# Kernel tuning notes

Measured on AMD Instinct MI355X. Metric: run time of the kernel, lower is better.

## Reference

```python
import jax, jax.numpy as jnp
import numpy as np

N = 50000      # nodes
E = 800000     # edges (before self loops)
NF = 4         # node feature dim
EF = 4         # edge feature dim
EMB = 16       # joint embedding dim
HID = 64       # hidden dim
OUT = 128      # output dim
H = 4          # heads (layers 0,1); last layer has 1 head
NEG_SLOPE = 0.2


def setup_inputs() -> dict:
    key = jax.random.key(0)
    ks = jax.random.split(key, 20)
    in0 = NF + EMB  # 20

    def lin(k, o, i):
        return (jax.random.normal(k, (o, i), jnp.float32) * np.float32(1.0 / np.sqrt(i)))

    return {
        'x': jax.random.normal(ks[0], (N, NF), jnp.float32),
        'edge_index': jax.random.randint(ks[1], (2, E), 0, N, dtype=jnp.int32),
        'edge_attr': jax.random.normal(ks[2], (E, EF), jnp.float32),
        'joint_types': jax.random.randint(ks[3], (N,), 0, 17, dtype=jnp.int32),
        'emb_table': jax.random.normal(ks[4], (17, EMB), jnp.float32) * 0.1,
        'W0': lin(ks[5], H * HID, in0),
        'a_src0': jax.random.normal(ks[6], (H, HID), jnp.float32) * 0.1,
        'a_dst0': jax.random.normal(ks[7], (H, HID), jnp.float32) * 0.1,
        'We0': lin(ks[8], H, EF),
        'W1': lin(ks[9], H * HID, HID),
        'a_src1': jax.random.normal(ks[10], (H, HID), jnp.float32) * 0.1,
        'a_dst1': jax.random.normal(ks[11], (H, HID), jnp.float32) * 0.1,
        'We1': lin(ks[12], H, EF),
        'W2': lin(ks[13], 1 * OUT, HID),
        'a_src2': jax.random.normal(ks[14], (1, OUT), jnp.float32) * 0.1,
        'a_dst2': jax.random.normal(ks[15], (1, OUT), jnp.float32) * 0.1,
        'We2': lin(ks[16], 1, EF),
    }


def gat_layer(x, src, dst, eattr, W, a_src, a_dst, We, num_nodes):
    # x: [N, F_in]; W: [H*C, F_in]; a_src/a_dst: [H, C]; We: [H, EF]
    Hh, C = a_src.shape
    h = (x @ W.T).reshape(num_nodes, Hh, C)  # [N, H, C]
    # per-node attention scores, gathered per edge (same math as per-edge dot)
    s_i = jnp.einsum('nhc,hc->nh', h, a_src)  # applied to x_i = x[dst]
    s_j = jnp.einsum('nhc,hc->nh', h, a_dst)  # applied to x_j = x[src]
    alpha = s_i[dst] + s_j[src] + eattr @ We.T  # [Etot, H]
    alpha = jax.nn.leaky_relu(alpha, NEG_SLOPE)
    # faithful to torch.softmax(alpha, dim=0): GLOBAL softmax over all edges per head
    alpha = jax.nn.softmax(alpha, axis=0)
    msgs = h[src] * alpha[:, :, None]  # [Etot, H, C]
    out = jax.ops.segment_sum(msgs, dst, num_segments=num_nodes)  # aggr='add'
    return out.mean(axis=1)  # update(): mean over heads -> [N, C]


def reference(x, edge_index, edge_attr, joint_types, emb_table,
              W0, a_src0, a_dst0, We0,
              W1, a_src1, a_dst1, We1,
              W2, a_src2, a_dst2, We2):
    num_nodes = x.shape[0]
    # add self loops (edge_attr fill 0.0)
    loops = jnp.arange(num_nodes, dtype=edge_index.dtype)
    src = jnp.concatenate([edge_index[0], loops])
    dst = jnp.concatenate([edge_index[1], loops])
    eattr = jnp.concatenate([edge_attr, jnp.zeros((num_nodes, edge_attr.shape[1]), edge_attr.dtype)], axis=0)

    h = jnp.concatenate([x, emb_table[joint_types]], axis=-1)  # [N, 20]
    h = gat_layer(h, src, dst, eattr, W0, a_src0, a_dst0, We0, num_nodes)
    h = jax.nn.elu(h)  # dropout is identity in eval mode
    h = gat_layer(h, src, dst, eattr, W1, a_src1, a_dst1, We1, num_nodes)
    h = jax.nn.elu(h)
    h = gat_layer(h, src, dst, eattr, W2, a_src2, a_dst2, We2, num_nodes)
    return h  # [N, OUT]
```

## Files before the change

kernel.cpp:

```cpp
#include <hip/hip_runtime.h>
#include <math.h>

#define NN 50000
#define EE 800000
#define EEN (EE+NN)
#define STRIDE 64
#define NFEAT 4
#define EFEAT 4
#define EMBD 16
#define IN0 20
#define HIDD 64
#define OUTD 128
#define EDGE_NB 1024

__device__ __forceinline__ unsigned short f2bf(float f){
  unsigned u = __float_as_uint(f);
  return (unsigned short)((u + 0x7FFFu + ((u>>16)&1u)) >> 16);
}
__device__ __forceinline__ float bfl(unsigned u){ return __uint_as_float(u<<16); }
__device__ __forceinline__ float bfh(unsigned u){ return __uint_as_float(u & 0xFFFF0000u); }

__device__ __forceinline__ unsigned f2h2(float a, float b){
  _Float16 ha=(_Float16)a, hb=(_Float16)b;
  unsigned short ua=*(unsigned short*)&ha, ub=*(unsigned short*)&hb;
  return (unsigned)ua | ((unsigned)ub<<16);
}
__device__ __forceinline__ float h2f(unsigned short u){
  _Float16 h=*(_Float16*)&u; return (float)h;
}

typedef unsigned uv4 __attribute__((ext_vector_type(4)));
typedef unsigned uv2 __attribute__((ext_vector_type(2)));
template<typename T>
__device__ __forceinline__ T ntload(const T* p){
  return __builtin_nontemporal_load(const_cast<T*>(p));
}

template<int V> struct ldt;
template<> struct ldt<4>{ using T = uint2; };
template<> struct ldt<2>{ using T = unsigned int; };

template<int F_IN,int HH,int CC>
__device__ __forceinline__ void av_one(const float* W, const float* asrc,
                                       const float* adst, float* av, int tid){
  if (tid >= HH*F_IN) return;
  int h = tid / F_IN, f = tid % F_IN;
  float s1=0.f, s2=0.f;
  for (int c=0;c<CC;c++){
    float wv = W[(size_t)(h*CC+c)*F_IN+f];
    s1 += asrc[h*CC+c]*wv;
    s2 += adst[h*CC+c]*wv;
  }
  av[tid] = s1;
  av[HH*F_IN+tid] = s2;
}
__global__ void k_av3(const float* W0, const float* as0, const float* ad0, float* av0,
                      const float* W1, const float* as1, const float* ad1, float* av1,
                      const float* W2, const float* as2, const float* ad2, float* av2,
                      float* zred, int* fill){
  int b = blockIdx.x, tid = threadIdx.x;
  if      (b==0){ av_one<IN0,4,64> (W0, as0, ad0, av0, tid); if (tid<192) zred[tid]=0.f; }
  else if (b==1)  av_one<64,4,64>  (W1, as1, ad1, av1, tid);
  else if (b==2)  av_one<64,1,128> (W2, as2, ad2, av2, tid);
  else { int i=(b-3)*256+tid; if (i<NN) fill[i]=0; }
}

__global__ void k_scatter(const int* __restrict__ ei, const float4* __restrict__ eattr,
                          int* fill, uv4* __restrict__ erec){
  int idx = blockIdx.x*blockDim.x + threadIdx.x;
  if (idx < EE){
    int d = ei[EE+idx];
    int s = ei[idx];
    float4 ea = eattr[idx];
    int pos = atomicAdd(&fill[d],1);
    int slot = d*STRIDE + 1 + pos;
    uv4 r; r.x=(unsigned)s; r.y=f2h2(ea.x,ea.y); r.z=f2h2(ea.z,ea.w); r.w=0u;
    erec[slot]=r;
  } else if (idx < EEN){
    int n = idx-EE;
    uv4 r; r.x=(unsigned)n; r.y=0u; r.z=0u; r.w=0u;
    erec[n*STRIDE]=r;
  }
}

template<int K,int NCOL,int HH,bool CONCAT>
__global__ __launch_bounds__(256)
void k_gemm(const float* __restrict__ xin, const int* __restrict__ jt,
            const float* __restrict__ emb, const float* __restrict__ W,
            const float* __restrict__ avp, unsigned short* __restrict__ hout,
            float* __restrict__ si, float* __restrict__ sj){
  constexpr int PITCH = 132;
  __shared__ float xT[K*PITCH];
  __shared__ float wT[K*PITCH];
  __shared__ float EMBL[CONCAT ? 17*EMBD : 1];
  int tid = threadIdx.x;
  int rbase = blockIdx.x*128, cbase = blockIdx.y*128;
  if (CONCAT){
    for (int i=tid; i<17*EMBD; i+=256) EMBL[i]=emb[i];
    __syncthreads();
    if (tid < 128){
      int row = tid;
      int gr = rbase+row; if (gr >= NN) gr = NN-1;
      float4 v = ((const float4*)xin)[gr];
      xT[0*PITCH+row]=v.x; xT[1*PITCH+row]=v.y;
      xT[2*PITCH+row]=v.z; xT[3*PITCH+row]=v.w;
      int j = jt[gr];
      #pragma unroll
      for (int k=0;k<EMBD;k++) xT[(NFEAT+k)*PITCH+row] = EMBL[j*EMBD+k];
    } else {
      int col = tid-128;
      const float4* wp = (const float4*)(W + (size_t)(cbase+col)*K);
      #pragma unroll
      for (int k4=0;k4<K/4;k4++){
        float4 v = wp[k4];
        wT[(4*k4+0)*PITCH+col]=v.x; wT[(4*k4+1)*PITCH+col]=v.y;
        wT[(4*k4+2)*PITCH+col]=v.z; wT[(4*k4+3)*PITCH+col]=v.w;
      }
    }
  } else {
    constexpr int K4 = K/4;
    for (int i=tid; i<128*K4; i+=256){
      int row = i/K4, k4 = i%K4;
      int gr = rbase+row; if (gr >= NN) gr = NN-1;
      float4 v = ((const float4*)xin)[(size_t)gr*K4 + k4];
      xT[(4*k4+0)*PITCH+row]=v.x; xT[(4*k4+1)*PITCH+row]=v.y;
      xT[(4*k4+2)*PITCH+row]=v.z; xT[(4*k4+3)*PITCH+row]=v.w;
    }
    for (int i=tid; i<128*K4; i+=256){
      int col = i/K4, k4 = i%K4;
      float4 v = ((const float4*)W)[(size_t)(cbase+col)*K4 + k4];
      wT[(4*k4+0)*PITCH+col]=v.x; wT[(4*k4+1)*PITCH+col]=v.y;
      wT[(4*k4+2)*PITCH+col]=v.z; wT[(4*k4+3)*PITCH+col]=v.w;
    }
  }
  __syncthreads();
  int lane = tid & 63, w = tid >> 6;
  int r0 = (w>>1)*64 + (lane&7)*8;
  int c0 = (w&1)*64 + (lane>>3)*8;
  float acc[8][8];
  #pragma unroll
  for (int i=0;i<8;i++)
    #pragma unroll
    for (int j=0;j<8;j++) acc[i][j]=0.f;
  #pragma unroll 4
  for (int k=0;k<K;k++){
    float a[8], b[8];
    *(float4*)&a[0] = *(const float4*)&xT[k*PITCH + r0];
    *(float4*)&a[4] = *(const float4*)&xT[k*PITCH + r0 + 4];
    *(float4*)&b[0] = *(const float4*)&wT[k*PITCH + c0];
    *(float4*)&b[4] = *(const float4*)&wT[k*PITCH + c0 + 4];
    #pragma unroll
    for (int i=0;i<8;i++)
      #pragma unroll
      for (int j=0;j<8;j++) acc[i][j] += a[i]*b[j];
  }
  if (blockIdx.y==0 && tid < 128){
    int row = tid, gr = rbase+row;
    if (gr < NN){
      #pragma unroll
      for (int h=0;h<HH;h++){
        float a=0.f, b=0.f;
        for (int k=0;k<K;k++){
          float xv = xT[k*PITCH+row];
          a += xv*avp[h*K+k];
          b += xv*avp[HH*K+h*K+k];
        }
        si[(size_t)gr*HH+h]=a;
        sj[(size_t)gr*HH+h]=b;
      }
    }
  }
  #pragma unroll
  for (int i=0;i<8;i++){
    int n = rbase + r0 + i;
    if (n < NN){
      uint4 o;
      o.x = (unsigned)f2bf(acc[i][0]) | ((unsigned)f2bf(acc[i][1])<<16);
      o.y = (unsigned)f2bf(acc[i][2]) | ((unsigned)f2bf(acc[i][3])<<16);
      o.z = (unsigned)f2bf(acc[i][4]) | ((unsigned)f2bf(acc[i][5])<<16);
      o.w = (unsigned)f2bf(acc[i][6]) | ((unsigned)f2bf(acc[i][7])<<16);
      *(uint4*)(hout + (size_t)n*NCOL + cbase + c0) = o;
    }
  }
}

template<int HH>
__global__ __launch_bounds__(256)
void k_edge2(const uv4* __restrict__ erec, const int* __restrict__ fill,
             const float* __restrict__ We, const float* __restrict__ si,
             const float* __restrict__ sj, unsigned* __restrict__ prec,
             float* __restrict__ zred){
  int wave = threadIdx.x>>6, lane = threadIdx.x&63;
  float z[HH];
  #pragma unroll
  for (int h=0;h<HH;h++) z[h]=0.f;
  for (int n = blockIdx.x*4 + wave; n < NN; n += EDGE_NB*4){
    int cnt = 1 + fill[n];
    if (lane < cnt){
      int slot = n*STRIDE + lane;
      uv4 r = ntload(&erec[slot]);
      int s = (int)r.x;
      float eax=h2f((unsigned short)(r.y&0xFFFFu)), eay=h2f((unsigned short)(r.y>>16));
      float eaz=h2f((unsigned short)(r.z&0xFFFFu)), eaw=h2f((unsigned short)(r.z>>16));
      if constexpr (HH==4){
        float4 siv = ((const float4*)si)[n];
        float4 sjv = ((const float4*)sj)[s];
        float te[4] = {siv.x+sjv.x, siv.y+sjv.y, siv.z+sjv.z, siv.w+sjv.w};
        float pv[4];
        #pragma unroll
        for (int h=0;h<4;h++){
          float t = te[h] + eax*We[h*EFEAT+0] + eay*We[h*EFEAT+1]
                          + eaz*We[h*EFEAT+2] + eaw*We[h*EFEAT+3];
          t = (t>0.f)? t : 0.2f*t;
          float p = expf(t);
          z[h]+=p; pv[h]=p;
        }
        uv4 o; o.x=f2h2(pv[0],pv[1]); o.y=f2h2(pv[2],pv[3]); o.z=(unsigned)s; o.w=0u;
        ((uv4*)prec)[slot] = o;
      } else {
        float t = si[n] + sj[s]
                + eax*We[0] + eay*We[1] + eaz*We[2] + eaw*We[3];
        t = (t>0.f)? t : 0.2f*t;
        float p = expf(t);
        z[0]+=p;
        uv2 o; o.x=__float_as_uint(p); o.y=(unsigned)s;
        ((uv2*)prec)[slot] = o;
      }
    }
  }
  __shared__ float zs[4][HH];
  #pragma unroll
  for (int h=0;h<HH;h++){
    float v=z[h];
    #pragma unroll
    for (int off=32; off>0; off>>=1) v += __shfl_xor(v,off,64);
    if (lane==0) zs[wave][h]=v;
  }
  __syncthreads();
  if (threadIdx.x < HH){
    float tot = zs[0][threadIdx.x]+zs[1][threadIdx.x]
              + zs[2][threadIdx.x]+zs[3][threadIdx.x];
    atomicAdd(&zred[threadIdx.x*16], tot);
  }
}

template<int HH,int CC,bool DO_ELU>
__global__ __launch_bounds__(256)
void k_agg(const unsigned short* __restrict__ hb, const unsigned* __restrict__ prec,
           const float* __restrict__ zred, const int* __restrict__ fill,
           float* __restrict__ outp){
  constexpr int HC = HH*CC;
  constexpr int V  = HC/64;
  using LT = typename ldt<V>::T;
  int wave = threadIdx.x>>6, lane = threadIdx.x&63;
  int n = blockIdx.x*4 + wave;
  int hd = (lane*V)/CC;
  int hw = hd>>1, hs = (hd&1)*16;
  float invZ = 1.0f/zred[hd*16];
  float acc[V];
  #pragma unroll
  for (int v=0;v<V;v++) acc[v]=0.f;
  auto mac = [&](float p, LT h){
    if constexpr (V==4){
      acc[0] += p*bfl(h.x); acc[1] += p*bfh(h.x);
      acc[2] += p*bfl(h.y); acc[3] += p*bfh(h.y);
    } else {
      acc[0] += p*bfl(h);   acc[1] += p*bfh(h);
    }
  };
  int beg = n*STRIDE, end = beg + 1 + fill[n];
  int i = beg;
  for (; i+8<=end; i+=8){
    int sr[8]; float p[8]; LT h[8];
    #pragma unroll
    for (int k=0;k<8;k++){
      if constexpr (HH==4){
        uint4 q = ((const uint4*)prec)[i+k];
        sr[k] = (int)q.z;
        unsigned wd = hw ? q.y : q.x;
        p[k] = h2f((unsigned short)(wd>>hs));
      } else {
        uint2 q = ((const uint2*)prec)[i+k];
        p[k] = __uint_as_float(q.x);
        sr[k] = (int)q.y;
      }
    }
    #pragma unroll
    for (int k=0;k<8;k++) h[k]=((const LT*)(hb + (size_t)sr[k]*HC))[lane];
    #pragma unroll
    for (int k=0;k<8;k++) mac(p[k], h[k]);
  }
  for (; i<end; i++){
    int sr; float p;
    if constexpr (HH==4){
      uint4 q = ((const uint4*)prec)[i];
      sr = (int)q.z;
      unsigned wd = hw ? q.y : q.x;
      p = h2f((unsigned short)(wd>>hs));
    } else {
      uint2 q = ((const uint2*)prec)[i];
      p = __uint_as_float(q.x);
      sr = (int)q.y;
    }
    LT h = ((const LT*)(hb + (size_t)sr*HC))[lane];
    mac(p, h);
  }
  #pragma unroll
  for (int v=0;v<V;v++) acc[v] *= invZ;
  if constexpr (HH==4){
    #pragma unroll
    for (int off=16; off<64; off<<=1){
      #pragma unroll
      for (int v=0;v<V;v++) acc[v] += __shfl_xor(acc[v], off, 64);
    }
    if (lane < 16){
      float4 o;
      o.x=0.25f*acc[0]; o.y=0.25f*acc[1]; o.z=0.25f*acc[2]; o.w=0.25f*acc[3];
      if (DO_ELU){
        o.x = (o.x>0.f)? o.x : expm1f(o.x);
        o.y = (o.y>0.f)? o.y : expm1f(o.y);
        o.z = (o.z>0.f)? o.z : expm1f(o.z);
        o.w = (o.w>0.f)? o.w : expm1f(o.w);
      }
      ((float4*)outp)[(size_t)n*(CC/4)+lane] = o;
    }
  } else {
    float2 o; o.x=acc[0]; o.y=acc[1];
    if (DO_ELU){
      o.x = (o.x>0.f)? o.x : expm1f(o.x);
      o.y = (o.y>0.f)? o.y : expm1f(o.y);
    }
    ((float2*)outp)[(size_t)n*(CC/2)+lane] = o;
  }
}

extern "C" void kernel_launch(void* const* d_in, const int* in_sizes, int n_in,
                              void* d_out, int out_size, void* d_ws, size_t ws_size,
                              hipStream_t stream){
  const float* x    = (const float*)d_in[0];
  const int*   ei   = (const int*)d_in[1];
  const float* eatt = (const float*)d_in[2];
  const int*   jt   = (const int*)d_in[3];
  const float* emb  = (const float*)d_in[4];
  const float* W0   = (const float*)d_in[5];
  const float* as0  = (const float*)d_in[6];
  const float* ad0  = (const float*)d_in[7];
  const float* We0  = (const float*)d_in[8];
  const float* W1   = (const float*)d_in[9];
  const float* as1  = (const float*)d_in[10];
  const float* ad1  = (const float*)d_in[11];
  const float* We1  = (const float*)d_in[12];
  const float* W2   = (const float*)d_in[13];
  const float* as2  = (const float*)d_in[14];
  const float* ad2  = (const float*)d_in[15];
  const float* We2  = (const float*)d_in[16];
  float* out = (float*)d_out;

  char* p = (char*)d_ws;
  auto alloc = [&](size_t bytes)->char*{
    char* r = p; p += (bytes + 255) & ~(size_t)255; return r;
  };
  unsigned short* hbuf = (unsigned short*)alloc((size_t)NN*256*2);
  float* x1     = (float*)alloc((size_t)NN*64*4);
  float* x2     = (float*)alloc((size_t)NN*64*4);
  float* si     = (float*)alloc((size_t)NN*4*4);
  float* sj     = (float*)alloc((size_t)NN*4*4);
  unsigned* prec= (unsigned*)alloc((size_t)NN*STRIDE*16);
  int*   fill   = (int*)alloc((size_t)NN*4);
  uv4*   erec   = (uv4*)alloc((size_t)NN*STRIDE*16);
  float* av0    = (float*)alloc(512*4);
  float* av1    = (float*)alloc(512*4);
  float* av2    = (float*)alloc(512*4);
  float* zred   = (float*)alloc(192*4);

  k_av3    <<<dim3(3+(NN+255)/256), 256, 0, stream>>>(W0,as0,ad0,av0, W1,as1,ad1,av1,
                                                      W2,as2,ad2,av2, zred, fill);
  k_scatter<<<dim3((EEN+255)/256),  256, 0, stream>>>(ei, (const float4*)eatt,
                                                      fill, erec);

  dim3 gg01((NN+127)/128, 2);
  dim3 gg2 ((NN+127)/128, 1);
  dim3 egrid2(EDGE_NB);
  dim3 ngrid(NN/4);

  k_gemm<IN0,256,4,true> <<<gg01, 256, 0, stream>>>(x, jt, emb, W0, av0, hbuf, si, sj);
  k_edge2<4>             <<<egrid2,256, 0, stream>>>(erec, fill, We0, si, sj, prec, zred+0);
  k_agg<4,64,true>       <<<ngrid,256, 0, stream>>>(hbuf, prec, zred+0, fill, x1);

  k_gemm<64,256,4,false> <<<gg01, 256, 0, stream>>>(x1, jt, emb, W1, av1, hbuf, si, sj);
  k_edge2<4>             <<<egrid2,256, 0, stream>>>(erec, fill, We1, si, sj, prec, zred+64);
  k_agg<4,64,true>       <<<ngrid,256, 0, stream>>>(hbuf, prec, zred+64, fill, x2);

  k_gemm<64,128,1,false> <<<gg2,  256, 0, stream>>>(x2, jt, emb, W2, av2, hbuf, si, sj);
  k_edge2<1>             <<<egrid2,256, 0, stream>>>(erec, fill, We2, si, sj, prec, zred+128);
  k_agg<1,128,false>     <<<ngrid,256, 0, stream>>>(hbuf, prec, zred+128, fill, out);
}
```

Before: 503.4 us.

## Launch one edge block per node group, spread softmax sums, deepen gather unroll

The edge-score kernel now launches one block per four nodes instead of a fixed 1024-block grid-stride loop. The global softmax denominators are accumulated into 32 padded partial slots per head to cut atomic contention, and the aggregation kernel sums those partials itself. The aggregation loop also gains a 16-wide unrolled gather stage so more neighbour-row loads are in flight at once. This launches many more small blocks and makes every aggregation wave perform 32 extra loads of the partial sums.

```diff
diff --git a/kernel.cpp b/kernel.cpp
--- a/kernel.cpp
+++ b/kernel.cpp
@@ -11,7 +11,7 @@
 #define IN0 20
 #define HIDD 64
 #define OUTD 128
-#define EDGE_NB 1024
+#define ZB 32
 
 __device__ __forceinline__ unsigned short f2bf(float f){
   unsigned u = __float_as_uint(f);
@@ -59,10 +59,14 @@
                       const float* W2, const float* as2, const float* ad2, float* av2,
                       float* zred, int* fill){
   int b = blockIdx.x, tid = threadIdx.x;
-  if      (b==0){ av_one<IN0,4,64> (W0, as0, ad0, av0, tid); if (tid<192) zred[tid]=0.f; }
-  else if (b==1)  av_one<64,4,64>  (W1, as1, ad1, av1, tid);
-  else if (b==2)  av_one<64,1,128> (W2, as2, ad2, av2, tid);
-  else { int i=(b-3)*256+tid; if (i<NN) fill[i]=0; }
+  if (b < 3){
+    for (int i=tid; i<2048; i+=256) zred[b*2048+i]=0.f;
+    if      (b==0) av_one<IN0,4,64> (W0, as0, ad0, av0, tid);
+    else if (b==1) av_one<64,4,64>  (W1, as1, ad1, av1, tid);
+    else           av_one<64,1,128> (W2, as2, ad2, av2, tid);
+  } else {
+    int i=(b-3)*256+tid; if (i<NN) fill[i]=0;
+  }
 }
 
 __global__ void k_scatter(const int* __restrict__ ei, const float4* __restrict__ eattr,
@@ -191,41 +195,40 @@
              const float* __restrict__ sj, unsigned* __restrict__ prec,
              float* __restrict__ zred){
   int wave = threadIdx.x>>6, lane = threadIdx.x&63;
+  int n = blockIdx.x*4 + wave;
   float z[HH];
   #pragma unroll
   for (int h=0;h<HH;h++) z[h]=0.f;
-  for (int n = blockIdx.x*4 + wave; n < NN; n += EDGE_NB*4){
-    int cnt = 1 + fill[n];
-    if (lane < cnt){
-      int slot = n*STRIDE + lane;
-      uv4 r = ntload(&erec[slot]);
-      int s = (int)r.x;
-      float eax=h2f((unsigned short)(r.y&0xFFFFu)), eay=h2f((unsigned short)(r.y>>16));
-      float eaz=h2f((unsigned short)(r.z&0xFFFFu)), eaw=h2f((unsigned short)(r.z>>16));
-      if constexpr (HH==4){
-        float4 siv = ((const float4*)si)[n];
-        float4 sjv = ((const float4*)sj)[s];
-        float te[4] = {siv.x+sjv.x, siv.y+sjv.y, siv.z+sjv.z, siv.w+sjv.w};
-        float pv[4];
-        #pragma unroll
-        for (int h=0;h<4;h++){
-          float t = te[h] + eax*We[h*EFEAT+0] + eay*We[h*EFEAT+1]
-                          + eaz*We[h*EFEAT+2] + eaw*We[h*EFEAT+3];
-          t = (t>0.f)? t : 0.2f*t;
-          float p = expf(t);
-          z[h]+=p; pv[h]=p;
-        }
-        uv4 o; o.x=f2h2(pv[0],pv[1]); o.y=f2h2(pv[2],pv[3]); o.z=(unsigned)s; o.w=0u;
-        ((uv4*)prec)[slot] = o;
-      } else {
-        float t = si[n] + sj[s]
-                + eax*We[0] + eay*We[1] + eaz*We[2] + eaw*We[3];
+  int cnt = 1 + fill[n];
+  if (lane < cnt){
+    int slot = n*STRIDE + lane;
+    uv4 r = ntload(&erec[slot]);
+    int s = (int)r.x;
+    float eax=h2f((unsigned short)(r.y&0xFFFFu)), eay=h2f((unsigned short)(r.y>>16));
+    float eaz=h2f((unsigned short)(r.z&0xFFFFu)), eaw=h2f((unsigned short)(r.z>>16));
+    if constexpr (HH==4){
+      float4 siv = ((const float4*)si)[n];
+      float4 sjv = ((const float4*)sj)[s];
+      float te[4] = {siv.x+sjv.x, siv.y+sjv.y, siv.z+sjv.z, siv.w+sjv.w};
+      float pv[4];
+      #pragma unroll
+      for (int h=0;h<4;h++){
+        float t = te[h] + eax*We[h*EFEAT+0] + eay*We[h*EFEAT+1]
+                        + eaz*We[h*EFEAT+2] + eaw*We[h*EFEAT+3];
         t = (t>0.f)? t : 0.2f*t;
         float p = expf(t);
-        z[0]+=p;
-        uv2 o; o.x=__float_as_uint(p); o.y=(unsigned)s;
-        ((uv2*)prec)[slot] = o;
+        z[h]=p; pv[h]=p;
       }
+      uv4 o; o.x=f2h2(pv[0],pv[1]); o.y=f2h2(pv[2],pv[3]); o.z=(unsigned)s; o.w=0u;
+      ((uv4*)prec)[slot] = o;
+    } else {
+      float t = si[n] + sj[s]
+              + eax*We[0] + eay*We[1] + eaz*We[2] + eaw*We[3];
+      t = (t>0.f)? t : 0.2f*t;
+      float p = expf(t);
+      z[0]=p;
+      uv2 o; o.x=__float_as_uint(p); o.y=(unsigned)s;
+      ((uv2*)prec)[slot] = o;
     }
   }
   __shared__ float zs[4][HH];
@@ -240,7 +243,7 @@
   if (threadIdx.x < HH){
     float tot = zs[0][threadIdx.x]+zs[1][threadIdx.x]
               + zs[2][threadIdx.x]+zs[3][threadIdx.x];
-    atomicAdd(&zred[threadIdx.x*16], tot);
+    atomicAdd(&zred[threadIdx.x*512 + (blockIdx.x&(ZB-1))*16], tot);
   }
 }
 
@@ -256,7 +259,10 @@
   int n = blockIdx.x*4 + wave;
   int hd = (lane*V)/CC;
   int hw = hd>>1, hs = (hd&1)*16;
-  float invZ = 1.0f/zred[hd*16];
+  float zt = 0.f;
+  #pragma unroll
+  for (int b=0;b<ZB;b++) zt += zred[hd*512 + b*16];
+  float invZ = 1.0f/zt;
   float acc[V];
   #pragma unroll
   for (int v=0;v<V;v++) acc[v]=0.f;
@@ -268,40 +274,41 @@
       acc[0] += p*bfl(h);   acc[1] += p*bfh(h);
     }
   };
-  int beg = n*STRIDE, end = beg + 1 + fill[n];
-  int i = beg;
-  for (; i+8<=end; i+=8){
-    int sr[8]; float p[8]; LT h[8];
-    #pragma unroll
-    for (int k=0;k<8;k++){
-      if constexpr (HH==4){
-        uint4 q = ((const uint4*)prec)[i+k];
-        sr[k] = (int)q.z;
-        unsigned wd = hw ? q.y : q.x;
-        p[k] = h2f((unsigned short)(wd>>hs));
-      } else {
-        uint2 q = ((const uint2*)prec)[i+k];
-        p[k] = __uint_as_float(q.x);
-        sr[k] = (int)q.y;
-      }
-    }
-    #pragma unroll
-    for (int k=0;k<8;k++) h[k]=((const LT*)(hb + (size_t)sr[k]*HC))[lane];
-    #pragma unroll
-    for (int k=0;k<8;k++) mac(p[k], h[k]);
-  }
-  for (; i<end; i++){
-    int sr; float p;
+  auto ldrec = [&](int idx, int& sr, float& p){
     if constexpr (HH==4){
-      uint4 q = ((const uint4*)prec)[i];
+      uint4 q = ((const uint4*)prec)[idx];
       sr = (int)q.z;
       unsigned wd = hw ? q.y : q.x;
       p = h2f((unsigned short)(wd>>hs));
     } else {
-      uint2 q = ((const uint2*)prec)[i];
+      uint2 q = ((const uint2*)prec)[idx];
       p = __uint_as_float(q.x);
       sr = (int)q.y;
     }
+  };
+  int beg = n*STRIDE, end = beg + 1 + fill[n];
+  int i = beg;
+  for (; i+16<=end; i+=16){
+    int sr[16]; float p[16]; LT h[16];
+    #pragma unroll
+    for (int k=0;k<16;k++) ldrec(i+k, sr[k], p[k]);
+    #pragma unroll
+    for (int k=0;k<16;k++) h[k]=((const LT*)(hb + (size_t)sr[k]*HC))[lane];
+    #pragma unroll
+    for (int k=0;k<16;k++) mac(p[k], h[k]);
+  }
+  for (; i+8<=end; i+=8){
+    int sr[8]; float p[8]; LT h[8];
+    #pragma unroll
+    for (int k=0;k<8;k++) ldrec(i+k, sr[k], p[k]);
+    #pragma unroll
+    for (int k=0;k<8;k++) h[k]=((const LT*)(hb + (size_t)sr[k]*HC))[lane];
+    #pragma unroll
+    for (int k=0;k<8;k++) mac(p[k], h[k]);
+  }
+  for (; i<end; i++){
+    int sr; float p;
+    ldrec(i, sr, p);
     LT h = ((const LT*)(hb + (size_t)sr*HC))[lane];
     mac(p, h);
   }
@@ -371,7 +378,7 @@
   float* av0    = (float*)alloc(512*4);
   float* av1    = (float*)alloc(512*4);
   float* av2    = (float*)alloc(512*4);
-  float* zred   = (float*)alloc(192*4);
+  float* zred   = (float*)alloc(3*2048*4);
 
   k_av3    <<<dim3(3+(NN+255)/256), 256, 0, stream>>>(W0,as0,ad0,av0, W1,as1,ad1,av1,
                                                       W2,as2,ad2,av2, zred, fill);
@@ -380,18 +387,17 @@
 
   dim3 gg01((NN+127)/128, 2);
   dim3 gg2 ((NN+127)/128, 1);
-  dim3 egrid2(EDGE_NB);
   dim3 ngrid(NN/4);
 
   k_gemm<IN0,256,4,true> <<<gg01, 256, 0, stream>>>(x, jt, emb, W0, av0, hbuf, si, sj);
-  k_edge2<4>             <<<egrid2,256, 0, stream>>>(erec, fill, We0, si, sj, prec, zred+0);
+  k_edge2<4>             <<<ngrid,256, 0, stream>>>(erec, fill, We0, si, sj, prec, zred+0);
   k_agg<4,64,true>       <<<ngrid,256, 0, stream>>>(hbuf, prec, zred+0, fill, x1);
 
   k_gemm<64,256,4,false> <<<gg01, 256, 0, stream>>>(x1, jt, emb, W1, av1, hbuf, si, sj);
-  k_edge2<4>             <<<egrid2,256, 0, stream>>>(erec, fill, We1, si, sj, prec, zred+64);
-  k_agg<4,64,true>       <<<ngrid,256, 0, stream>>>(hbuf, prec, zred+64, fill, x2);
+  k_edge2<4>             <<<ngrid,256, 0, stream>>>(erec, fill, We1, si, sj, prec, zred+2048);
+  k_agg<4,64,true>       <<<ngrid,256, 0, stream>>>(hbuf, prec, zred+2048, fill, x2);
 
   k_gemm<64,128,1,false> <<<gg2,  256, 0, stream>>>(x2, jt, emb, W2, av2, hbuf, si, sj);
-  k_edge2<1>             <<<egrid2,256, 0, stream>>>(erec, fill, We2, si, sj, prec, zred+128);
-  k_agg<1,128,false>     <<<ngrid,256, 0, stream>>>(hbuf, prec, zred+128, fill, out);
-}
+  k_edge2<1>             <<<ngrid,256, 0, stream>>>(erec, fill, We2, si, sj, prec, zred+4096);
+  k_agg<1,128,false>     <<<ngrid,256, 0, stream>>>(hbuf, prec, zred+4096, fill, out);
+}
```

Result: no change. 506.3 us (+0.6%).
